# Kernel optimization log

Measured on AMD Instinct MI355X. Metric: run time of the kernel, lower is better.

The kernel has to match this reference:

```python
import jax, jax.numpy as jnp
import numpy as np

DIM = 1024
HEADS = 16
DIM_HEAD = 64
INNER = HEADS * DIM_HEAD  # 1024


def setup_inputs() -> dict:
    key = jax.random.key(0)
    k1, k2, k3, k4 = jax.random.split(key, 4)
    x = jax.random.normal(k1, (4, 2048, DIM), dtype=jnp.float32)
    # nn.Linear(dim, 3*inner, bias=False): weight (3*inner, dim); store transposed (dim, 3*inner)
    w_qkv = jax.random.normal(k2, (DIM, 3 * INNER), dtype=jnp.float32) * (DIM ** -0.5)
    # nn.Linear(inner, dim) with bias
    w_out = jax.random.normal(k3, (INNER, DIM), dtype=jnp.float32) * (INNER ** -0.5)
    b_out = jax.random.normal(k4, (DIM,), dtype=jnp.float32) * 0.01
    return {"x": x, "w_qkv": w_qkv, "w_out": w_out, "b_out": b_out}


def reference(x, w_qkv, w_out, b_out):
    b, n, _ = x.shape
    scale = DIM_HEAD ** -0.5
    qkv = x @ w_qkv  # [b, n, 3*inner]
    q, k, v = jnp.split(qkv, 3, axis=-1)
    # 'b n (h d) -> b h n d'
    def split_heads(t):
        return t.reshape(b, n, HEADS, DIM_HEAD).transpose(0, 2, 1, 3)
    q, k, v = split_heads(q), split_heads(k), split_heads(v)
    sim = jnp.einsum('bhid,bhjd->bhij', q, k) * scale  # [b, h, n, n]
    attn = jax.nn.softmax(sim, axis=-1)
    out = jnp.einsum('bhij,bhjd->bhid', attn, v)  # [b, h, n, d]
    out = out.transpose(0, 2, 1, 3).reshape(b, n, INNER)  # 'b h n d -> b n (h d)'
    return out @ w_out + b_out
```

## Files before the change

kernel.cpp:

```cpp
#include <hip/hip_runtime.h>
#include <hip/hip_bf16.h>

#define BATCH 4
#define SEQ   2048
#define DIM   1024
#define HEADS 16
#define DHEAD 64
#define INNER 1024
#define QKV_N 3072

typedef short bf16x8 __attribute__((ext_vector_type(8)));
typedef float f32x4  __attribute__((ext_vector_type(4)));
#define MFMA16(a,b,c) __builtin_amdgcn_mfma_f32_16x16x32_bf16((a),(b),(c),0,0,0)

#define QSCALE 0.1803368801111204f

static __device__ __forceinline__ unsigned fau(float f) { return __float_as_uint(f); }

static __device__ __forceinline__ uint2 pack_hi4(float4 v) {
    return make_uint2((fau(v.x) >> 16) | (fau(v.y) & 0xffff0000u),
                      (fau(v.z) >> 16) | (fau(v.w) & 0xffff0000u));
}
static __device__ __forceinline__ float4 resid4(float4 v) {
    float4 r;
    r.x = v.x - __uint_as_float(fau(v.x) & 0xffff0000u);
    r.y = v.y - __uint_as_float(fau(v.y) & 0xffff0000u);
    r.z = v.z - __uint_as_float(fau(v.z) & 0xffff0000u);
    r.w = v.w - __uint_as_float(fau(v.w) & 0xffff0000u);
    return r;
}
static __device__ __forceinline__ uint2 pack_lo4(float4 v) { return pack_hi4(resid4(v)); }

static __device__ __forceinline__ unsigned cvt_pk_bf16(float a, float b) {
    unsigned r;
    asm("v_cvt_pk_bf16_f32 %0, %1, %2" : "=v"(r) : "v"(a), "v"(b));
    return r;
}

static __device__ __forceinline__ void gemm_core(const float* __restrict__ A,
                                                 const float* __restrict__ B,
                                                 unsigned short* As,
                                                 unsigned short* Bs,
                                                 f32x4 (&acc)[4][4],
                                                 int N, int K, int row0, int col0)
{
    const int tid  = threadIdx.x;
    const int lane = tid & 63;
    const int w    = tid >> 6;
    const int l15  = lane & 15;
    const int g    = lane >> 4;
    const int wr   = w >> 1, wc = w & 1;

    for (int k0 = 0; k0 < K; k0 += 32) {
        __syncthreads();
        #pragma unroll
        for (int p = 0; p < 4; ++p) {
            const int m  = p * 32 + (tid >> 3);
            const int kq = (tid & 7) * 4;
            const float4 v = *(const float4*)&A[(size_t)(row0 + m) * K + k0 + kq];
            const int sw = (m & 7) << 3;
            *(uint2*)&As[m * 64 + (kq ^ sw)]        = pack_hi4(v);
            *(uint2*)&As[m * 64 + ((32 + kq) ^ sw)] = pack_lo4(v);
        }
        #pragma unroll
        for (int p = 0; p < 4; ++p) {
            const int n  = tid & 127;
            const int kb = p * 8 + (tid >> 7) * 4;
            float4 v;
            v.x = B[(size_t)(k0 + kb + 0) * N + col0 + n];
            v.y = B[(size_t)(k0 + kb + 1) * N + col0 + n];
            v.z = B[(size_t)(k0 + kb + 2) * N + col0 + n];
            v.w = B[(size_t)(k0 + kb + 3) * N + col0 + n];
            const int sw = (n & 7) << 3;
            *(uint2*)&Bs[n * 64 + (kb ^ sw)]        = pack_hi4(v);
            *(uint2*)&Bs[n * 64 + ((32 + kb) ^ sw)] = pack_lo4(v);
        }
        __syncthreads();

        bf16x8 ah[4], al[4], bh[4], bl[4];
        #pragma unroll
        for (int mt = 0; mt < 4; ++mt) {
            const int m = wr * 64 + mt * 16 + l15;
            const int sw = (m & 7) << 3;
            ah[mt] = *(bf16x8*)&As[m * 64 + ((g * 8) ^ sw)];
            al[mt] = *(bf16x8*)&As[m * 64 + ((32 + g * 8) ^ sw)];
        }
        #pragma unroll
        for (int nt = 0; nt < 4; ++nt) {
            const int n = wc * 64 + nt * 16 + l15;
            const int sw = (n & 7) << 3;
            bh[nt] = *(bf16x8*)&Bs[n * 64 + ((g * 8) ^ sw)];
            bl[nt] = *(bf16x8*)&Bs[n * 64 + ((32 + g * 8) ^ sw)];
        }
        #pragma unroll
        for (int mt = 0; mt < 4; ++mt)
            #pragma unroll
            for (int nt = 0; nt < 4; ++nt) {
                acc[mt][nt] = MFMA16(ah[mt], bh[nt], acc[mt][nt]);
                acc[mt][nt] = MFMA16(ah[mt], bl[nt], acc[mt][nt]);
                acc[mt][nt] = MFMA16(al[mt], bh[nt], acc[mt][nt]);
            }
    }
}

__global__ __launch_bounds__(256, 2) void gemm_bf16x3(const float* __restrict__ A,
                                                      const float* __restrict__ B,
                                                      const float* __restrict__ bias,
                                                      float* __restrict__ C,
                                                      int M, int N, int K)
{
    __shared__ unsigned short As[128 * 64];
    __shared__ unsigned short Bs[128 * 64];

    const int tid  = threadIdx.x;
    const int lane = tid & 63;
    const int w    = tid >> 6;
    const int l15  = lane & 15;
    const int g    = lane >> 4;
    const int wr   = w >> 1, wc = w & 1;
    const int row0 = blockIdx.y * 128, col0 = blockIdx.x * 128;

    f32x4 acc[4][4] = {};
    gemm_core(A, B, As, Bs, acc, N, K, row0, col0);

    #pragma unroll
    for (int nt = 0; nt < 4; ++nt) {
        const int c = col0 + wc * 64 + nt * 16 + l15;
        const float bv = bias ? bias[c] : 0.f;
        #pragma unroll
        for (int mt = 0; mt < 4; ++mt)
            #pragma unroll
            for (int r = 0; r < 4; ++r) {
                const int rr = row0 + wr * 64 + mt * 16 + g * 4 + r;
                C[(size_t)rr * N + c] = acc[mt][nt][r] + bv;
            }
    }
}

__global__ __launch_bounds__(256, 2) void gemm_qkv(const float* __restrict__ A,
                                                   const float* __restrict__ B,
                                                   unsigned short* __restrict__ q_hl,
                                                   unsigned short* __restrict__ k_hl,
                                                   unsigned short* __restrict__ vt,
                                                   int N, int K)
{
    __shared__ unsigned short As[128 * 64];
    __shared__ unsigned short Bs[128 * 64];

    const int tid  = threadIdx.x;
    const int lane = tid & 63;
    const int w    = tid >> 6;
    const int l15  = lane & 15;
    const int g    = lane >> 4;
    const int wr   = w >> 1, wc = w & 1;
    const int row0 = blockIdx.y * 128, col0 = blockIdx.x * 128;

    f32x4 acc[4][4] = {};
    gemm_core(A, B, As, Bs, acc, N, K, row0, col0);

    if (col0 < 2 * INNER) {
        unsigned short* plane = (col0 < INNER) ? q_hl : k_hl;
        const float sc = (col0 < INNER) ? QSCALE : 1.0f;
        #pragma unroll
        for (int nt = 0; nt < 4; ++nt) {
            const int c  = col0 + wc * 64 + nt * 16 + l15;
            const int cc = c & (INNER - 1);
            const int hd = (cc >> 6) * 128 + (cc & 63);
            #pragma unroll
            for (int mt = 0; mt < 4; ++mt)
                #pragma unroll
                for (int r = 0; r < 4; ++r) {
                    const int rr = row0 + wr * 64 + mt * 16 + g * 4 + r;
                    const float v = acc[mt][nt][r] * sc;
                    const unsigned u = fau(v);
                    const float res = v - __uint_as_float(u & 0xffff0000u);
                    unsigned short* dp = plane + (size_t)rr * 2048 + hd;
                    dp[0]  = (unsigned short)(u >> 16);
                    dp[64] = (unsigned short)(fau(res) >> 16);
                }
        }
    } else {
        #pragma unroll
        for (int nt = 0; nt < 4; ++nt) {
            const int f = col0 + wc * 64 + nt * 16 + l15 - 2 * INNER;
            #pragma unroll
            for (int mt = 0; mt < 4; ++mt) {
                const int rr0 = row0 + wr * 64 + mt * 16 + g * 4;
                const int bb  = rr0 >> 11;
                const int n   = rr0 & (SEQ - 1);
                const int pn  = (n & ~31) | ((n & 12) << 1) | ((n & 16) >> 2);
                const uint2 pk = make_uint2(
                    cvt_pk_bf16(acc[mt][nt][0], acc[mt][nt][1]),
                    cvt_pk_bf16(acc[mt][nt][2], acc[mt][nt][3]));
                *(uint2*)&vt[((size_t)bb * INNER + f) * SEQ + pn] = pk;
            }
        }
    }
}

__global__ __launch_bounds__(256, 2) void attn_mfma(const unsigned short* __restrict__ q_hl,
                                                    const unsigned short* __restrict__ k_hl,
                                                    const unsigned short* __restrict__ vt,
                                                    float* __restrict__ attn_out)
{
    __shared__ unsigned short Ks[64 * 128];
    __shared__ unsigned short Vs[64 * 64];

    const int tid  = threadIdx.x;
    const int lane = tid & 63;
    const int w    = tid >> 6;
    const int l15  = lane & 15;
    const int g    = lane >> 4;
    const int qb = blockIdx.x, h = blockIdx.y, b = blockIdx.z;
    const int q0 = qb * 256 + w * 64;

    bf16x8 qh[4][2], ql[4][2];
    #pragma unroll
    for (int qs = 0; qs < 4; ++qs) {
        const unsigned short* qp =
            q_hl + (size_t)(b * SEQ + q0 + qs * 16 + l15) * 2048 + h * 128;
        #pragma unroll
        for (int kk = 0; kk < 2; ++kk) {
            qh[qs][kk] = *(const bf16x8*)&qp[kk * 32 + g * 8];
            ql[qs][kk] = *(const bf16x8*)&qp[64 + kk * 32 + g * 8];
        }
    }

    f32x4 o[4][4] = {};
    float m_run[4] = {-1e30f, -1e30f, -1e30f, -1e30f};
    float l_run[4] = {0.f, 0.f, 0.f, 0.f};

    const int kj   = tid >> 4;
    const int ko8  = (tid & 15) * 8;
    const int kdst = kj * 128 + (ko8 ^ (kj << 3));
    const unsigned short* ksrc =
        k_hl + ((size_t)(b * SEQ + kj)) * 2048 + h * 128 + ko8;

    const int vd   = tid >> 3;
    const int vu8  = (tid & 7) * 8;
    const int vdst = vd * 64 + (vu8 ^ ((vd & 7) << 3));
    const unsigned short* vsrc =
        vt + ((size_t)(b * HEADS + h) * 64 + vd) * SEQ + vu8;

    const int krow = l15 * 128;
    int koff[2][2];
    #pragma unroll
    for (int kk = 0; kk < 2; ++kk) {
        koff[kk][0] = (kk * 32 + g * 8) ^ (l15 * 8);
        koff[kk][1] = (64 + kk * 32 + g * 8) ^ (l15 * 8);
    }
    const int vrow = l15 * 64;
    const int voff[2] = { (g * 8) ^ ((l15 & 7) * 8), (32 + g * 8) ^ ((l15 & 7) * 8) };

    for (int kv = 0; kv < SEQ / 64; ++kv) {
        const int j0 = kv * 64;
        __syncthreads();
        #pragma unroll
        for (int p = 0; p < 4; ++p)
            *(bf16x8*)&Ks[p * 2048 + kdst] =
                *(const bf16x8*)&ksrc[(size_t)(j0 + p * 16) * 2048];
        #pragma unroll
        for (int p = 0; p < 2; ++p)
            *(bf16x8*)&Vs[p * 2048 + vdst] =
                *(const bf16x8*)&vsrc[(size_t)p * 32 * SEQ + j0];
        __syncthreads();

        f32x4 s[4][4] = {};
        #pragma unroll
        for (int jt = 0; jt < 4; ++jt) {
            #pragma unroll
            for (int kk = 0; kk < 2; ++kk) {
                const bf16x8 khf = *(const bf16x8*)&Ks[jt * 2048 + krow + koff[kk][0]];
                const bf16x8 klf = *(const bf16x8*)&Ks[jt * 2048 + krow + koff[kk][1]];
                #pragma unroll
                for (int qs = 0; qs < 4; ++qs) {
                    s[qs][jt] = MFMA16(khf, qh[qs][kk], s[qs][jt]);
                    s[qs][jt] = MFMA16(khf, ql[qs][kk], s[qs][jt]);
                    s[qs][jt] = MFMA16(klf, qh[qs][kk], s[qs][jt]);
                }
            }
        }

        bf16x8 pav[4][2];
        #pragma unroll
        for (int qs = 0; qs < 4; ++qs) {
            float mx = -1e30f;
            #pragma unroll
            for (int jt = 0; jt < 4; ++jt)
                #pragma unroll
                for (int r = 0; r < 4; ++r) mx = fmaxf(mx, s[qs][jt][r]);
            mx = fmaxf(mx, __shfl_xor(mx, 16));
            mx = fmaxf(mx, __shfl_xor(mx, 32));
            if (!__all(mx - m_run[qs] <= 8.f)) {
                const float mnew = fmaxf(m_run[qs], mx);
                const float corr = __builtin_amdgcn_exp2f(m_run[qs] - mnew);
                m_run[qs] = mnew;
                l_run[qs] *= corr;
                const float cr0 = __shfl(corr, g * 4 + 0);
                const float cr1 = __shfl(corr, g * 4 + 1);
                const float cr2 = __shfl(corr, g * 4 + 2);
                const float cr3 = __shfl(corr, g * 4 + 3);
                #pragma unroll
                for (int nt = 0; nt < 4; ++nt) {
                    o[qs][nt][0] *= cr0; o[qs][nt][1] *= cr1;
                    o[qs][nt][2] *= cr2; o[qs][nt][3] *= cr3;
                }
            }
            float sm = 0.f;
            #pragma unroll
            for (int jt = 0; jt < 4; ++jt)
                #pragma unroll
                for (int r = 0; r < 4; ++r) {
                    const float e = __builtin_amdgcn_exp2f(s[qs][jt][r] - m_run[qs]);
                    s[qs][jt][r] = e; sm += e;
                }
            sm += __shfl_xor(sm, 16);
            sm += __shfl_xor(sm, 32);
            l_run[qs] += sm;

            #pragma unroll
            for (int t = 0; t < 2; ++t) {
                union { uint2 u[2]; bf16x8 v; } P;
                P.u[0] = make_uint2(cvt_pk_bf16(s[qs][2 * t][0],     s[qs][2 * t][1]),
                                    cvt_pk_bf16(s[qs][2 * t][2],     s[qs][2 * t][3]));
                P.u[1] = make_uint2(cvt_pk_bf16(s[qs][2 * t + 1][0], s[qs][2 * t + 1][1]),
                                    cvt_pk_bf16(s[qs][2 * t + 1][2], s[qs][2 * t + 1][3]));
                pav[qs][t] = P.v;
            }
        }

        #pragma unroll
        for (int t = 0; t < 2; ++t)
            #pragma unroll
            for (int nt = 0; nt < 4; ++nt) {
                const bf16x8 vb = *(const bf16x8*)&Vs[nt * 1024 + vrow + voff[t]];
                #pragma unroll
                for (int qs = 0; qs < 4; ++qs)
                    o[qs][nt] = MFMA16(pav[qs][t], vb, o[qs][nt]);
            }
    }

    #pragma unroll
    for (int qs = 0; qs < 4; ++qs) {
        const float il = 1.f / l_run[qs];
        const float n0 = __shfl(il, g * 4 + 0);
        const float n1 = __shfl(il, g * 4 + 1);
        const float n2 = __shfl(il, g * 4 + 2);
        const float n3 = __shfl(il, g * 4 + 3);
        #pragma unroll
        for (int nt = 0; nt < 4; ++nt) {
            float* op = attn_out +
                (size_t)(b * SEQ + q0 + qs * 16 + g * 4) * INNER + h * DHEAD + nt * 16 + l15;
            op[0 * INNER] = o[qs][nt][0] * n0;
            op[1 * INNER] = o[qs][nt][1] * n1;
            op[2 * INNER] = o[qs][nt][2] * n2;
            op[3 * INNER] = o[qs][nt][3] * n3;
        }
    }
}

extern "C" void kernel_launch(void* const* d_in, const int* in_sizes, int n_in,
                              void* d_out, int out_size, void* d_ws, size_t ws_size,
                              hipStream_t stream)
{
    const float* x     = (const float*)d_in[0];
    const float* w_qkv = (const float*)d_in[1];
    const float* w_out = (const float*)d_in[2];
    const float* b_out = (const float*)d_in[3];
    float* out = (float*)d_out;

    const int M = BATCH * SEQ;

    unsigned short* q_hl = (unsigned short*)d_ws;
    unsigned short* k_hl = q_hl + (size_t)M * 2048;
    unsigned short* vt   = k_hl + (size_t)M * 2048;
    float* attn_out = (float*)(vt + (size_t)BATCH * INNER * SEQ);

    gemm_qkv<<<dim3(QKV_N / 128, M / 128), 256, 0, stream>>>(
        x, w_qkv, q_hl, k_hl, vt, QKV_N, DIM);

    attn_mfma<<<dim3(SEQ / 256, HEADS, BATCH), 256, 0, stream>>>(
        q_hl, k_hl, vt, attn_out);

    gemm_bf16x3<<<dim3(INNER / 128, M / 128), 256, 0, stream>>>(
        attn_out, w_out, b_out, out, M, INNER, DIM);
}
```

Before: 382.6 us.

## Pre-pack GEMM operands into swizzled bf16 hi/lo tiles with register prefetch

Adds pack kernels that convert x, w_qkv and w_out into a tiled, pre-swizzled bf16 hi/lo layout. The GEMM core can then copy whole 16-byte chunks straight into LDS, with the next tile prefetched into registers. The attention kernel now writes its output directly in the packed layout, so the output projection skips the fp32 round trip and the repeated split. The point is to remove per-block conversion work and the strided, uncoalesced B loads from the GEMM inner loops. The cost is three extra kernel launches, extra workspace traffic for the packed copies, and 2-byte scattered stores at the end of attention.

```diff
diff --git a/kernel.cpp b/kernel.cpp
--- a/kernel.cpp
+++ b/kernel.cpp
@@ -8,6 +8,7 @@
 #define DHEAD 64
 #define INNER 1024
 #define QKV_N 3072
+#define MTOT  8192
 
 typedef short bf16x8 __attribute__((ext_vector_type(8)));
 typedef float f32x4  __attribute__((ext_vector_type(4)));
@@ -37,12 +38,57 @@
     return r;
 }
 
-static __device__ __forceinline__ void gemm_core(const float* __restrict__ A,
-                                                 const float* __restrict__ B,
-                                                 unsigned short* As,
-                                                 unsigned short* Bs,
-                                                 f32x4 (&acc)[4][4],
-                                                 int N, int K, int row0, int col0)
+__global__ __launch_bounds__(256) void pack_rows_hl(const float* __restrict__ src,
+                                                    unsigned short* __restrict__ dst,
+                                                    int Mtot, int K)
+{
+    const int m = blockIdx.x * 256 + threadIdx.x;
+    const int t = blockIdx.y;
+    const float* sp = src + (size_t)m * K + t * 32;
+    unsigned short buf[64];
+    #pragma unroll
+    for (int i = 0; i < 32; i += 4) {
+        const float4 v = *(const float4*)&sp[i];
+        *(uint2*)&buf[i]      = pack_hi4(v);
+        *(uint2*)&buf[32 + i] = pack_lo4(v);
+    }
+    unsigned short* dp = dst + ((size_t)t * Mtot + m) * 64;
+    const int s7 = m & 7;
+    #pragma unroll
+    for (int G = 0; G < 8; ++G)
+        *(bf16x8*)&dp[(G ^ s7) * 8] = *(bf16x8*)&buf[G * 8];
+}
+
+__global__ __launch_bounds__(256) void pack_cols_hl(const float* __restrict__ src,
+                                                    unsigned short* __restrict__ dst,
+                                                    int Ntot)
+{
+    const int n = blockIdx.x * 256 + threadIdx.x;
+    const int t = blockIdx.y;
+    float vals[32];
+    #pragma unroll
+    for (int i = 0; i < 32; ++i) vals[i] = src[(size_t)(t * 32 + i) * Ntot + n];
+    unsigned short buf[64];
+    #pragma unroll
+    for (int i = 0; i < 32; i += 4) {
+        const float4 v = make_float4(vals[i], vals[i + 1], vals[i + 2], vals[i + 3]);
+        *(uint2*)&buf[i]      = pack_hi4(v);
+        *(uint2*)&buf[32 + i] = pack_lo4(v);
+    }
+    unsigned short* dp = dst + ((size_t)t * Ntot + n) * 64;
+    const int s7 = n & 7;
+    #pragma unroll
+    for (int G = 0; G < 8; ++G)
+        *(bf16x8*)&dp[(G ^ s7) * 8] = *(bf16x8*)&buf[G * 8];
+}
+
+static __device__ __forceinline__ void gemm_core_pk(const unsigned short* __restrict__ Ap,
+                                                    const unsigned short* __restrict__ Bp,
+                                                    unsigned short* As,
+                                                    unsigned short* Bs,
+                                                    f32x4 (&acc)[4][4],
+                                                    int Mtot, int Ntot, int NT,
+                                                    int row0, int col0)
 {
     const int tid  = threadIdx.x;
     const int lane = tid & 63;
@@ -51,46 +97,61 @@
     const int g    = lane >> 4;
     const int wr   = w >> 1, wc = w & 1;
 
-    for (int k0 = 0; k0 < K; k0 += 32) {
+    const unsigned short* aSrc = Ap + (size_t)row0 * 64 + tid * 8;
+    const unsigned short* bSrc = Bp + (size_t)col0 * 64 + tid * 8;
+    const size_t aStep = (size_t)Mtot * 64;
+    const size_t bStep = (size_t)Ntot * 64;
+
+    int aoff[4][2], boff[4][2];
+    #pragma unroll
+    for (int mt = 0; mt < 4; ++mt) {
+        const int m = wr * 64 + mt * 16 + l15;
+        const int sw = (m & 7) << 3;
+        aoff[mt][0] = m * 64 + ((g * 8) ^ sw);
+        aoff[mt][1] = m * 64 + ((32 + g * 8) ^ sw);
+    }
+    #pragma unroll
+    for (int nt = 0; nt < 4; ++nt) {
+        const int n = wc * 64 + nt * 16 + l15;
+        const int sw = (n & 7) << 3;
+        boff[nt][0] = n * 64 + ((g * 8) ^ sw);
+        boff[nt][1] = n * 64 + ((32 + g * 8) ^ sw);
+    }
+
+    bf16x8 ar[4], br[4];
+    #pragma unroll
+    for (int p = 0; p < 4; ++p) {
+        ar[p] = *(const bf16x8*)(aSrc + p * 2048);
+        br[p] = *(const bf16x8*)(bSrc + p * 2048);
+    }
+
+    for (int t = 0; t < NT; ++t) {
         __syncthreads();
         #pragma unroll
         for (int p = 0; p < 4; ++p) {
-            const int m  = p * 32 + (tid >> 3);
-            const int kq = (tid & 7) * 4;
-            const float4 v = *(const float4*)&A[(size_t)(row0 + m) * K + k0 + kq];
-            const int sw = (m & 7) << 3;
-            *(uint2*)&As[m * 64 + (kq ^ sw)]        = pack_hi4(v);
-            *(uint2*)&As[m * 64 + ((32 + kq) ^ sw)] = pack_lo4(v);
-        }
-        #pragma unroll
-        for (int p = 0; p < 4; ++p) {
-            const int n  = tid & 127;
-            const int kb = p * 8 + (tid >> 7) * 4;
-            float4 v;
-            v.x = B[(size_t)(k0 + kb + 0) * N + col0 + n];
-            v.y = B[(size_t)(k0 + kb + 1) * N + col0 + n];
-            v.z = B[(size_t)(k0 + kb + 2) * N + col0 + n];
-            v.w = B[(size_t)(k0 + kb + 3) * N + col0 + n];
-            const int sw = (n & 7) << 3;
-            *(uint2*)&Bs[n * 64 + (kb ^ sw)]        = pack_hi4(v);
-            *(uint2*)&Bs[n * 64 + ((32 + kb) ^ sw)] = pack_lo4(v);
+            *(bf16x8*)&As[tid * 8 + p * 2048] = ar[p];
+            *(bf16x8*)&Bs[tid * 8 + p * 2048] = br[p];
         }
         __syncthreads();
-
+        if (t + 1 < NT) {
+            const unsigned short* a2 = aSrc + (size_t)(t + 1) * aStep;
+            const unsigned short* b2 = bSrc + (size_t)(t + 1) * bStep;
+            #pragma unroll
+            for (int p = 0; p < 4; ++p) {
+                ar[p] = *(const bf16x8*)(a2 + p * 2048);
+                br[p] = *(const bf16x8*)(b2 + p * 2048);
+            }
+        }
         bf16x8 ah[4], al[4], bh[4], bl[4];
         #pragma unroll
         for (int mt = 0; mt < 4; ++mt) {
-            const int m = wr * 64 + mt * 16 + l15;
-            const int sw = (m & 7) << 3;
-            ah[mt] = *(bf16x8*)&As[m * 64 + ((g * 8) ^ sw)];
-            al[mt] = *(bf16x8*)&As[m * 64 + ((32 + g * 8) ^ sw)];
+            ah[mt] = *(const bf16x8*)&As[aoff[mt][0]];
+            al[mt] = *(const bf16x8*)&As[aoff[mt][1]];
         }
         #pragma unroll
         for (int nt = 0; nt < 4; ++nt) {
-            const int n = wc * 64 + nt * 16 + l15;
-            const int sw = (n & 7) << 3;
-            bh[nt] = *(bf16x8*)&Bs[n * 64 + ((g * 8) ^ sw)];
-            bl[nt] = *(bf16x8*)&Bs[n * 64 + ((32 + g * 8) ^ sw)];
+            bh[nt] = *(const bf16x8*)&Bs[boff[nt][0]];
+            bl[nt] = *(const bf16x8*)&Bs[boff[nt][1]];
         }
         #pragma unroll
         for (int mt = 0; mt < 4; ++mt)
@@ -103,11 +164,10 @@
     }
 }
 
-__global__ __launch_bounds__(256, 2) void gemm_bf16x3(const float* __restrict__ A,
-                                                      const float* __restrict__ B,
+__global__ __launch_bounds__(256, 2) void gemm_out_pk(const unsigned short* __restrict__ Ap,
+                                                      const unsigned short* __restrict__ Bp,
                                                       const float* __restrict__ bias,
-                                                      float* __restrict__ C,
-                                                      int M, int N, int K)
+                                                      float* __restrict__ C)
 {
     __shared__ unsigned short As[128 * 64];
     __shared__ unsigned short Bs[128 * 64];
@@ -121,28 +181,27 @@
     const int row0 = blockIdx.y * 128, col0 = blockIdx.x * 128;
 
     f32x4 acc[4][4] = {};
-    gemm_core(A, B, As, Bs, acc, N, K, row0, col0);
+    gemm_core_pk(Ap, Bp, As, Bs, acc, MTOT, INNER, 32, row0, col0);
 
     #pragma unroll
     for (int nt = 0; nt < 4; ++nt) {
         const int c = col0 + wc * 64 + nt * 16 + l15;
-        const float bv = bias ? bias[c] : 0.f;
+        const float bv = bias[c];
         #pragma unroll
         for (int mt = 0; mt < 4; ++mt)
             #pragma unroll
             for (int r = 0; r < 4; ++r) {
                 const int rr = row0 + wr * 64 + mt * 16 + g * 4 + r;
-                C[(size_t)rr * N + c] = acc[mt][nt][r] + bv;
-            }
-    }
-}
-
-__global__ __launch_bounds__(256, 2) void gemm_qkv(const float* __restrict__ A,
-                                                   const float* __restrict__ B,
-                                                   unsigned short* __restrict__ q_hl,
-                                                   unsigned short* __restrict__ k_hl,
-                                                   unsigned short* __restrict__ vt,
-                                                   int N, int K)
+                C[(size_t)rr * INNER + c] = acc[mt][nt][r] + bv;
+            }
+    }
+}
+
+__global__ __launch_bounds__(256, 2) void gemm_qkv_pk(const unsigned short* __restrict__ Ap,
+                                                      const unsigned short* __restrict__ Bp,
+                                                      unsigned short* __restrict__ q_hl,
+                                                      unsigned short* __restrict__ k_hl,
+                                                      unsigned short* __restrict__ vt)
 {
     __shared__ unsigned short As[128 * 64];
     __shared__ unsigned short Bs[128 * 64];
@@ -156,7 +215,7 @@
     const int row0 = blockIdx.y * 128, col0 = blockIdx.x * 128;
 
     f32x4 acc[4][4] = {};
-    gemm_core(A, B, As, Bs, acc, N, K, row0, col0);
+    gemm_core_pk(Ap, Bp, As, Bs, acc, MTOT, QKV_N, 32, row0, col0);
 
     if (col0 < 2 * INNER) {
         unsigned short* plane = (col0 < INNER) ? q_hl : k_hl;
@@ -201,7 +260,7 @@
 __global__ __launch_bounds__(256, 2) void attn_mfma(const unsigned short* __restrict__ q_hl,
                                                     const unsigned short* __restrict__ k_hl,
                                                     const unsigned short* __restrict__ vt,
-                                                    float* __restrict__ attn_out)
+                                                    unsigned short* __restrict__ ao_hl)
 {
     __shared__ unsigned short Ks[64 * 128];
     __shared__ unsigned short Vs[64 * 64];
@@ -343,18 +402,29 @@
     #pragma unroll
     for (int qs = 0; qs < 4; ++qs) {
         const float il = 1.f / l_run[qs];
-        const float n0 = __shfl(il, g * 4 + 0);
-        const float n1 = __shfl(il, g * 4 + 1);
-        const float n2 = __shfl(il, g * 4 + 2);
-        const float n3 = __shfl(il, g * 4 + 3);
+        const float nr0 = __shfl(il, g * 4 + 0);
+        const float nr1 = __shfl(il, g * 4 + 1);
+        const float nr2 = __shfl(il, g * 4 + 2);
+        const float nr3 = __shfl(il, g * 4 + 3);
+        const float nr[4] = {nr0, nr1, nr2, nr3};
         #pragma unroll
         for (int nt = 0; nt < 4; ++nt) {
-            float* op = attn_out +
-                (size_t)(b * SEQ + q0 + qs * 16 + g * 4) * INNER + h * DHEAD + nt * 16 + l15;
-            op[0 * INNER] = o[qs][nt][0] * n0;
-            op[1 * INNER] = o[qs][nt][1] * n1;
-            op[2 * INNER] = o[qs][nt][2] * n2;
-            op[3 * INNER] = o[qs][nt][3] * n3;
+            const int k  = h * DHEAD + nt * 16 + l15;
+            const int t  = k >> 5;
+            const int kk = k & 31;
+            const int G  = kk >> 3;
+            const int e  = kk & 7;
+            #pragma unroll
+            for (int r = 0; r < 4; ++r) {
+                const int M  = b * SEQ + q0 + qs * 16 + g * 4 + r;
+                const int s7 = M & 7;
+                unsigned short* dp = ao_hl + ((size_t)t * MTOT + M) * 64;
+                const float v = o[qs][nt][r] * nr[r];
+                const unsigned u = fau(v);
+                const float res = v - __uint_as_float(u & 0xffff0000u);
+                dp[((G ^ s7) << 3) + e]       = (unsigned short)(u >> 16);
+                dp[(((G + 4) ^ s7) << 3) + e] = (unsigned short)(fau(res) >> 16);
+            }
         }
     }
 }
@@ -369,19 +439,23 @@
     const float* b_out = (const float*)d_in[3];
     float* out = (float*)d_out;
 
-    const int M = BATCH * SEQ;
-
-    unsigned short* q_hl = (unsigned short*)d_ws;
-    unsigned short* k_hl = q_hl + (size_t)M * 2048;
-    unsigned short* vt   = k_hl + (size_t)M * 2048;
-    float* attn_out = (float*)(vt + (size_t)BATCH * INNER * SEQ);
-
-    gemm_qkv<<<dim3(QKV_N / 128, M / 128), 256, 0, stream>>>(
-        x, w_qkv, q_hl, k_hl, vt, QKV_N, DIM);
+    unsigned short* q_hl  = (unsigned short*)d_ws;
+    unsigned short* k_hl  = q_hl  + (size_t)MTOT * 2048;
+    unsigned short* vt    = k_hl  + (size_t)MTOT * 2048;
+    unsigned short* xa_hl = vt    + (size_t)BATCH * INNER * SEQ;
+    unsigned short* wq_hl = xa_hl + (size_t)32 * MTOT * 64;
+    unsigned short* wo_hl = wq_hl + (size_t)32 * QKV_N * 64;
+
+    pack_rows_hl<<<dim3(MTOT / 256, 32), 256, 0, stream>>>(x, xa_hl, MTOT, DIM);
+    pack_cols_hl<<<dim3(QKV_N / 256, 32), 256, 0, stream>>>(w_qkv, wq_hl, QKV_N);
+    pack_cols_hl<<<dim3(INNER / 256, 32), 256, 0, stream>>>(w_out, wo_hl, INNER);
+
+    gemm_qkv_pk<<<dim3(QKV_N / 128, MTOT / 128), 256, 0, stream>>>(
+        xa_hl, wq_hl, q_hl, k_hl, vt);
 
     attn_mfma<<<dim3(SEQ / 256, HEADS, BATCH), 256, 0, stream>>>(
-        q_hl, k_hl, vt, attn_out);
-
-    gemm_bf16x3<<<dim3(INNER / 128, M / 128), 256, 0, stream>>>(
-        attn_out, w_out, b_out, out, M, INNER, DIM);
-}
+        q_hl, k_hl, vt, xa_hl);
+
+    gemm_out_pk<<<dim3(INNER / 128, MTOT / 128), 256, 0, stream>>>(
+        xa_hl, wo_hl, b_out, out);
+}
```

Result: faster. 362.6 us (-5.2%).
